# Kernel optimization log

Measured on AMD Instinct MI355X. Metric: run time of the kernel, lower is better.

Reference implementation:

```python
import jax, jax.numpy as jnp
import numpy as np

DIM = 512
NUM_HEADS = 8
HEAD_DIM = DIM // NUM_HEADS
SCALE = HEAD_DIM ** -0.5
HIDDEN = int(DIM * 4.0)
LN_EPS = 1e-5


def layer_norm(x, w, b):
    mu = jnp.mean(x, axis=-1, keepdims=True)
    var = jnp.var(x, axis=-1, keepdims=True)
    return (x - mu) * jax.lax.rsqrt(var + LN_EPS) * w + b


def setup_inputs() -> dict:
    key = jax.random.key(0)
    ks = jax.random.split(key, 8)
    s = 0.02
    return {
        "x": jax.random.normal(ks[0], (8, 4096, DIM), dtype=jnp.float32),
        "ln1_w": jnp.ones((DIM,), jnp.float32),
        "ln1_b": jnp.zeros((DIM,), jnp.float32),
        "qkv_w": jax.random.normal(ks[1], (3 * DIM, DIM), jnp.float32) * s,
        "proj_w": jax.random.normal(ks[2], (DIM, DIM), jnp.float32) * s,
        "proj_b": jnp.zeros((DIM,), jnp.float32),
        "ln2_w": jnp.ones((DIM,), jnp.float32),
        "ln2_b": jnp.zeros((DIM,), jnp.float32),
        "fc1_w": jax.random.normal(ks[3], (HIDDEN, DIM), jnp.float32) * s,
        "fc1_b": jnp.zeros((HIDDEN,), jnp.float32),
        "fc2_w": jax.random.normal(ks[4], (DIM, HIDDEN), jnp.float32) * s,
        "fc2_b": jnp.zeros((DIM,), jnp.float32),
        "eca_w": jax.random.normal(ks[5], (1, 1, 3), jnp.float32) * 0.5,
    }


def channel_attention(x, qkv_w, proj_w, proj_b):
    B, N, C = x.shape
    qkv = (x @ qkv_w.T).reshape(B, N, 3, NUM_HEADS, HEAD_DIM)
    qkv = qkv.transpose(2, 0, 3, 1, 4)  # (3, B, h, N, hd)
    q, k, v = qkv[0], qkv[1] * SCALE, qkv[2]
    # cross-covariance attention: (hd x hd) per head
    attn = jax.nn.softmax(jnp.einsum("bhnd,bhne->bhde", k, v), axis=-1)
    out = jnp.einsum("bhde,bhne->bhnd", attn, q)  # (B, h, N, hd)
    out = out.transpose(0, 2, 1, 3).reshape(B, N, C)
    return out @ proj_w.T + proj_b


def mlp_eca(x, fc1_w, fc1_b, fc2_w, fc2_b, eca_w):
    B, N, C = x.shape
    H = W = int(np.sqrt(N))
    h = jax.nn.gelu(x @ fc1_w.T + fc1_b, approximate=False)
    y = h @ fc2_w.T + fc2_b  # (B, N, C)
    # faithful replication of torch .view(B, C, H, W) on contiguous (B, N, C)
    y4 = y.reshape(B, C, H, W)
    pooled = jnp.mean(y4, axis=(2, 3))  # (B, C)
    conv = jax.lax.conv_general_dilated(
        pooled[:, None, :], eca_w, window_strides=(1,), padding=[(1, 1)],
        dimension_numbers=("NCW", "OIW", "NCW"))[:, 0, :]  # (B, C)
    gate = jax.nn.sigmoid(conv)[:, :, None, None]
    y4 = y4 * gate + y4
    return y4.reshape(B, C, H * W).transpose(0, 2, 1)  # (B, N, C)


def reference(x, ln1_w, ln1_b, qkv_w, proj_w, proj_b, ln2_w, ln2_b,
              fc1_w, fc1_b, fc2_w, fc2_b, eca_w):
    cur = layer_norm(x, ln1_w, ln1_b)
    x = x + channel_attention(cur, qkv_w, proj_w, proj_b)
    x = x + mlp_eca(layer_norm(x, ln2_w, ln2_b), fc1_w, fc1_b, fc2_w, fc2_b, eca_w)
    return x
```

## Files before the change

### kernel.cpp

```cpp
#include <hip/hip_runtime.h>
#include <hip/hip_bf16.h>

typedef __bf16 bf16;
typedef __bf16 bf16x8 __attribute__((ext_vector_type(8)));
typedef float floatx4 __attribute__((ext_vector_type(4)));

#define B_    8
#define N_    4096
#define C_    512
#define BN_   32768
#define HID_  2048
#define SCALE_ 0.125f

__device__ __forceinline__ void load_lds16(const void* g, void* l) {
    __builtin_amdgcn_global_load_lds(
        (const __attribute__((address_space(1))) void*)g,
        (__attribute__((address_space(3))) void*)l, 16, 0, 0);
}

__global__ void sniff_kernel(const unsigned int* __restrict__ xw, int* __restrict__ flag)
{
    int t = threadIdx.x;
    int votes = 0;
#pragma unroll
    for (int i = 0; i < 4; i++) {
        unsigned w = xw[t * 4 + i];
        if (w == 0u) continue;
        unsigned a = w & 0xFFFFu;
        unsigned e = (a >> 7) & 0xFFu;
        if (a != 0u && e >= 110u && e <= 135u) votes++; else votes--;
    }
#pragma unroll
    for (int off = 32; off; off >>= 1) votes += __shfl_xor(votes, off);
    __shared__ int s[4];
    if ((t & 63) == 0) s[t >> 6] = votes;
    __syncthreads();
    if (t == 0) *flag = (s[0] + s[1] + s[2] + s[3]) > 0 ? 1 : 0;
}

struct ConvArgs {
    const void* src[12];
    unsigned    dstoff[12];
    int         n[12];
};

__global__ __launch_bounds__(256) void convert_params(
    ConvArgs args, char* __restrict__ ws, const int* __restrict__ flag)
{
    int seg = blockIdx.y;
    int n = args.n[seg];
    int base = blockIdx.x * 2048;
    if (base >= n) return;
    bf16* dst = (bf16*)(ws + args.dstoff[seg]);
    const void* src = args.src[seg];
    bool isbf = (*flag != 0);
#pragma unroll
    for (int j = 0; j < 8; j++) {
        int idx = base + threadIdx.x + j * 256;
        if (idx < n) {
            float v = isbf ? (float)((const bf16*)src)[idx]
                           : ((const float*)src)[idx];
            dst[idx] = (bf16)v;
        }
    }
}

__global__ __launch_bounds__(256) void ln_dyn_kernel(
    const void* __restrict__ xv, const bf16* __restrict__ w,
    const bf16* __restrict__ b, bf16* __restrict__ out, const int* __restrict__ flag)
{
    int wave = threadIdx.x >> 6, lane = threadIdx.x & 63;
    size_t row = (size_t)blockIdx.x * 4 + wave;
    float f[8];
    if (*flag) {
        bf16x8 v = *(const bf16x8*)((const bf16*)xv + row * C_ + lane * 8);
#pragma unroll
        for (int j = 0; j < 8; j++) f[j] = (float)v[j];
    } else {
        const float4* p = (const float4*)((const float*)xv + row * C_ + lane * 8);
        float4 v0 = p[0], v1 = p[1];
        f[0]=v0.x; f[1]=v0.y; f[2]=v0.z; f[3]=v0.w;
        f[4]=v1.x; f[5]=v1.y; f[6]=v1.z; f[7]=v1.w;
    }
    float s = 0.f, sq = 0.f;
#pragma unroll
    for (int j = 0; j < 8; j++) { s += f[j]; sq += f[j]*f[j]; }
#pragma unroll
    for (int off = 32; off; off >>= 1) { s += __shfl_xor(s, off); sq += __shfl_xor(sq, off); }
    float mean = s * (1.f/512.f);
    float var  = sq * (1.f/512.f) - mean*mean;
    float inv  = rsqrtf(var + 1e-5f);
    bf16x8 wv = *(const bf16x8*)(w + lane*8);
    bf16x8 bv = *(const bf16x8*)(b + lane*8);
    bf16x8 o;
#pragma unroll
    for (int j = 0; j < 8; j++) o[j] = (bf16)((f[j]-mean)*inv*(float)wv[j] + (float)bv[j]);
    *(bf16x8*)(out + row * C_ + lane*8) = o;
}

__global__ __launch_bounds__(256) void ln_f32_kernel(
    const float* __restrict__ x, const bf16* __restrict__ w,
    const bf16* __restrict__ b, bf16* __restrict__ out)
{
    int wave = threadIdx.x >> 6, lane = threadIdx.x & 63;
    size_t row = (size_t)blockIdx.x * 4 + wave;
    const float4* p = (const float4*)(x + row * C_ + lane * 8);
    float4 v0 = p[0], v1 = p[1];
    float f[8] = { v0.x, v0.y, v0.z, v0.w, v1.x, v1.y, v1.z, v1.w };
    float s = 0.f, sq = 0.f;
#pragma unroll
    for (int j = 0; j < 8; j++) { s += f[j]; sq += f[j]*f[j]; }
#pragma unroll
    for (int off = 32; off; off >>= 1) { s += __shfl_xor(s, off); sq += __shfl_xor(sq, off); }
    float mean = s * (1.f/512.f);
    float var  = sq * (1.f/512.f) - mean*mean;
    float inv  = rsqrtf(var + 1e-5f);
    bf16x8 wv = *(const bf16x8*)(w + lane*8);
    bf16x8 bv = *(const bf16x8*)(b + lane*8);
    bf16x8 o;
#pragma unroll
    for (int j = 0; j < 8; j++) o[j] = (bf16)((f[j]-mean)*inv*(float)wv[j] + (float)bv[j]);
    *(bf16x8*)(out + row * C_ + lane*8) = o;
}

enum { EPI_NONE = 0, EPI_BIAS = 1, EPI_BIAS_RESID = 2, EPI_BIAS_GELU = 3, EPI_QKV = 4 };

template<typename OutT, int EPI>
__global__ __launch_bounds__(256, 2) void gemm_bt(
    const bf16* __restrict__ A, const bf16* __restrict__ W,
    const bf16* __restrict__ bias, const void* __restrict__ resid,
    const int* __restrict__ flag,
    OutT* __restrict__ Cout, bf16* __restrict__ Cout2, int M, int Nn, int K)
{
    __shared__ bf16 As[128][32];
    __shared__ bf16 Bs[128][32];
    const int t = threadIdx.x;
    const int wave = t >> 6, lane = t & 63;
    const int quad = lane >> 4, l16 = lane & 15;
    const int m0 = blockIdx.y * 128, n0 = blockIdx.x * 128;
    const int wm = (wave & 1) * 64, wn = (wave >> 1) * 64;
    floatx4 acc[4][4] = {};

    for (int k0 = 0; k0 < K; k0 += 32) {
#pragma unroll
        for (int i = 0; i < 2; i++) {
            int chunk = i * 256 + t;
            int row = chunk >> 2, kc = (chunk & 3) * 8;
            load_lds16(&A[(size_t)(m0 + row) * K + k0 + kc], &As[row][kc]);
            load_lds16(&W[(size_t)(n0 + row) * K + k0 + kc], &Bs[row][kc]);
        }
        __syncthreads();
        bf16x8 af[4], bfr[4];
#pragma unroll
        for (int mi = 0; mi < 4; mi++) af[mi]  = *(const bf16x8*)&As[wm + mi*16 + l16][quad*8];
#pragma unroll
        for (int ni = 0; ni < 4; ni++) bfr[ni] = *(const bf16x8*)&Bs[wn + ni*16 + l16][quad*8];
#pragma unroll
        for (int mi = 0; mi < 4; mi++)
#pragma unroll
            for (int ni = 0; ni < 4; ni++)
                acc[mi][ni] = __builtin_amdgcn_mfma_f32_16x16x32_bf16(af[mi], bfr[ni], acc[mi][ni], 0, 0, 0);
        __syncthreads();
    }

    size_t ldc = (size_t)Nn; int csub = 0; bool to2 = false;
    if (EPI == EPI_QKV) {
        if (n0 >= 512) { to2 = true; ldc = 1024; csub = 512; }
        else           { ldc = 512; }
    }
    bool isbf = false;
    if (EPI == EPI_BIAS_RESID) isbf = (*flag != 0);

#pragma unroll
    for (int mi = 0; mi < 4; mi++) {
#pragma unroll
        for (int ni = 0; ni < 4; ni++) {
            int col = n0 + wn + ni*16 + l16;
            float bv = (EPI == EPI_BIAS || EPI == EPI_BIAS_RESID || EPI == EPI_BIAS_GELU)
                       ? (float)bias[col] : 0.f;
#pragma unroll
            for (int r = 0; r < 4; r++) {
                int rowg = m0 + wm + mi*16 + quad*4 + r;
                size_t idx = (size_t)rowg * ldc + (col - csub);
                float v = acc[mi][ni][r] + bv;
                if (EPI == EPI_BIAS_RESID) {
                    float rres = isbf ? (float)((const bf16*)resid)[idx]
                                      : ((const float*)resid)[idx];
                    v += rres;
                }
                if (EPI == EPI_BIAS_GELU)  v = 0.5f * v * (1.f + erff(v * 0.70710678118654752f));
                if (EPI == EPI_QKV && to2) Cout2[idx] = (bf16)v;
                else                       Cout[idx]  = (OutT)v;
            }
        }
    }
}

__global__ __launch_bounds__(256) void attn_logits_mfma(
    const bf16* __restrict__ kv, float* __restrict__ partial)
{
    __shared__ bf16 Kt[64][136];
    __shared__ bf16 Vt[64][136];
    int s = blockIdx.x, bh = blockIdx.y, b = bh >> 3, h = bh & 7;
    int t = threadIdx.x, wave = t >> 6, lane = t & 63;
    int quad = lane >> 4, l16 = lane & 15;
    floatx4 acc[4] = {};
    for (int c = 0; c < 8; c++) {
        int n0 = s * 1024 + c * 128;
        {
            int isv = t >> 7;
            int r   = t & 127;
            const bf16* gp = &kv[((size_t)b * N_ + n0 + r) * 1024 + h * 64 + isv * 512];
            bf16x8 rowv[8];
#pragma unroll
            for (int u = 0; u < 8; u++) rowv[u] = *(const bf16x8*)(gp + u * 8);
            bf16 (*dst)[136] = isv ? Vt : Kt;
#pragma unroll
            for (int u = 0; u < 8; u++)
#pragma unroll
                for (int j = 0; j < 8; j++)
                    dst[u * 8 + j][r] = rowv[u][j];
        }
        __syncthreads();
#pragma unroll
        for (int ks = 0; ks < 4; ks++) {
            bf16x8 af = *(const bf16x8*)&Kt[wave * 16 + l16][ks * 32 + quad * 8];
#pragma unroll
            for (int ni = 0; ni < 4; ni++) {
                bf16x8 bfv = *(const bf16x8*)&Vt[ni * 16 + l16][ks * 32 + quad * 8];
                acc[ni] = __builtin_amdgcn_mfma_f32_16x16x32_bf16(af, bfv, acc[ni], 0, 0, 0);
            }
        }
        __syncthreads();
    }
    float* p = partial + ((size_t)bh * 4 + s) * 4096;
#pragma unroll
    for (int ni = 0; ni < 4; ni++)
#pragma unroll
        for (int r = 0; r < 4; r++)
            p[(wave * 16 + quad * 4 + r) * 64 + ni * 16 + l16] = acc[ni][r];
}

__global__ __launch_bounds__(256) void attn_softmax_kernel(
    const float* __restrict__ partial, bf16* __restrict__ attnb)
{
    int bh = blockIdx.x;
    int wave = threadIdx.x >> 6, lane = threadIdx.x & 63;
    for (int r = 0; r < 16; r++) {
        int d = wave * 16 + r;
        float v = 0.f;
#pragma unroll
        for (int s = 0; s < 4; s++) v += partial[((size_t)bh*4 + s)*4096 + d*64 + lane];
        v *= SCALE_;
        float m = v;
#pragma unroll
        for (int off = 32; off; off >>= 1) m = fmaxf(m, __shfl_xor(m, off));
        float p = expf(v - m);
        float sum = p;
#pragma unroll
        for (int off = 32; off; off >>= 1) sum += __shfl_xor(sum, off);
        attnb[(size_t)bh*4096 + d*64 + lane] = (bf16)(p / sum);
    }
}

__global__ __launch_bounds__(256) void attn_apply_mfma(
    const bf16* __restrict__ q, const bf16* __restrict__ attnb,
    bf16* __restrict__ outT)
{
    int bh = blockIdx.y, b = bh >> 3, h = bh & 7;
    int t = threadIdx.x, wave = t >> 6, lane = t & 63;
    int quad = lane >> 4, l16 = lane & 15;
    int nbase = blockIdx.x * 256 + wave * 64;
    bf16x8 bfrag[4][2];
#pragma unroll
    for (int di = 0; di < 4; di++)
#pragma unroll
        for (int ks = 0; ks < 2; ks++)
            bfrag[di][ks] = *(const bf16x8*)&attnb[(size_t)bh*4096 + (di*16 + l16)*64 + ks*32 + quad*8];
    floatx4 acc[4][4] = {};
#pragma unroll
    for (int mi = 0; mi < 4; mi++) {
#pragma unroll
        for (int ks = 0; ks < 2; ks++) {
            bf16x8 af = *(const bf16x8*)&q[((size_t)b*N_ + nbase + mi*16 + l16)*512 + h*64 + ks*32 + quad*8];
#pragma unroll
            for (int di = 0; di < 4; di++)
                acc[mi][di] = __builtin_amdgcn_mfma_f32_16x16x32_bf16(af, bfrag[di][ks], acc[mi][di], 0, 0, 0);
        }
    }
#pragma unroll
    for (int mi = 0; mi < 4; mi++)
#pragma unroll
        for (int di = 0; di < 4; di++)
#pragma unroll
            for (int r = 0; r < 4; r++)
                outT[((size_t)b*N_ + nbase + mi*16 + quad*4 + r)*512 + h*64 + di*16 + l16] =
                    (bf16)acc[mi][di][r];
}

__global__ __launch_bounds__(256) void pooled_kernel(
    const bf16* __restrict__ y, float* __restrict__ pooled)
{
    int bc = blockIdx.x;
    const bf16* p = y + (size_t)bc * 4096 + threadIdx.x * 16;
    float s = 0.f;
#pragma unroll
    for (int i = 0; i < 2; i++) {
        bf16x8 v = *(const bf16x8*)(p + i*8);
#pragma unroll
        for (int j = 0; j < 8; j++) s += (float)v[j];
    }
#pragma unroll
    for (int off = 32; off; off >>= 1) s += __shfl_xor(s, off);
    __shared__ float red[4];
    if ((threadIdx.x & 63) == 0) red[threadIdx.x >> 6] = s;
    __syncthreads();
    if (threadIdx.x == 0)
        pooled[bc] = (red[0] + red[1] + red[2] + red[3]) * (1.f/4096.f);
}

__global__ void gate_kernel(const float* __restrict__ pooled,
                            const bf16* __restrict__ eca_w, float* __restrict__ gate1)
{
    int c = threadIdx.x, b = blockIdx.x;
    float w0 = (float)eca_w[0], w1 = (float)eca_w[1], w2 = (float)eca_w[2];
    const float* p = pooled + b * 512;
    float conv = w1 * p[c];
    if (c > 0)   conv += w0 * p[c-1];
    if (c < 511) conv += w2 * p[c+1];
    float g = 1.f / (1.f + expf(-conv));
    gate1[b * 512 + c] = 1.f + g;
}

__global__ __launch_bounds__(256) void final_kernel(
    const bf16* __restrict__ y, const float* __restrict__ gate1,
    float* __restrict__ out)
{
    int b = blockIdx.z, c0 = blockIdx.y * 64, n0 = blockIdx.x * 64;
    __shared__ float ytile[64][65];
    int t = threadIdx.x;
#pragma unroll
    for (int i = 0; i < 2; i++) {
        int chunk = t * 2 + i;
        int ci = chunk >> 3, nj = (chunk & 7) * 8;
        bf16x8 v = *(const bf16x8*)&y[(size_t)b * ((size_t)N_*C_) + (size_t)(c0+ci) * 4096 + n0 + nj];
#pragma unroll
        for (int j = 0; j < 8; j++) ytile[ci][nj+j] = (float)v[j];
    }
    __syncthreads();
    int cc = t & 63, nb = t >> 6;
    float g = gate1[b * 512 + c0 + cc];
    for (int p = 0; p < 16; p++) {
        int nr = p * 4 + nb;
        size_t idx = ((size_t)b * N_ + n0 + nr) * C_ + c0 + cc;
        out[idx] = out[idx] + g * ytile[cc][nr];
    }
}

extern "C" void kernel_launch(void* const* d_in, const int* in_sizes, int n_in,
                              void* d_out, int out_size, void* d_ws, size_t ws_size,
                              hipStream_t stream)
{
    float* outf = (float*)d_out;
    bf16*  outb = (bf16*)d_out;
    char* ws = (char*)d_ws;

    int*   flag    = (int*)ws;
    float* pooled  = (float*)(ws + 4096);
    float* gate1   = (float*)(ws + 20480);
    bf16* ln1_w = (bf16*)(ws + 65536);
    bf16* ln1_b = (bf16*)(ws + 67584);
    bf16* ln2_w = (bf16*)(ws + 69632);
    bf16* ln2_b = (bf16*)(ws + 71680);
    bf16* proj_b= (bf16*)(ws + 73728);
    bf16* fc2_b = (bf16*)(ws + 75776);
    bf16* eca_w = (bf16*)(ws + 77824);
    bf16* fc1_b = (bf16*)(ws + 81920);
    bf16* qkv_w = (bf16*)(ws + ((size_t)1 << 20));
    bf16* proj_w= (bf16*)(ws + (size_t)2621440);
    bf16* fc1_w = (bf16*)(ws + ((size_t)3 << 20));
    bf16* fc2_w = (bf16*)(ws + ((size_t)5 << 20));
    float* partial = (float*)(ws + ((size_t)7  << 20));
    bf16*  attnb   = (bf16*)(ws + ((size_t)11 << 20));
    bf16*  T1      = (bf16*)(ws + ((size_t)16 << 20));
    bf16*  kvbuf   = (bf16*)(ws + ((size_t)48 << 20));
    bf16*  hbuf    = kvbuf;

    sniff_kernel<<<1, 256, 0, stream>>>((const unsigned int*)d_in[0], flag);

    ConvArgs ca;
    const int   srcidx[12] = { 1, 2, 6, 7, 5, 11, 12, 9, 3, 4, 8, 10 };
    const unsigned offs[12] = { 65536, 67584, 69632, 71680, 73728, 75776, 77824, 81920,
                                1u<<20, 2621440u, 3u<<20, 5u<<20 };
    for (int i = 0; i < 12; i++) {
        ca.src[i] = d_in[srcidx[i]];
        ca.dstoff[i] = offs[i];
        ca.n[i] = in_sizes[srcidx[i]];
    }
    convert_params<<<dim3(512, 12), 256, 0, stream>>>(ca, ws, flag);

    ln_dyn_kernel<<<BN_/4, 256, 0, stream>>>(d_in[0], ln1_w, ln1_b, T1, flag);

    gemm_bt<bf16, EPI_QKV><<<dim3(12, 256), 256, 0, stream>>>(
        T1, qkv_w, nullptr, nullptr, flag, outb, kvbuf, BN_, 1536, 512);

    attn_logits_mfma<<<dim3(4, 64), 256, 0, stream>>>(kvbuf, partial);
    attn_softmax_kernel<<<64, 256, 0, stream>>>(partial, attnb);
    attn_apply_mfma<<<dim3(16, 64), 256, 0, stream>>>(outb, attnb, T1);

    gemm_bt<float, EPI_BIAS_RESID><<<dim3(4, 256), 256, 0, stream>>>(
        T1, proj_w, proj_b, d_in[0], flag, outf, nullptr, BN_, 512, 512);

    ln_f32_kernel<<<BN_/4, 256, 0, stream>>>(outf, ln2_w, ln2_b, T1);

    for (int ch = 0; ch < 2; ch++) {
        bf16* Tch = T1 + (size_t)ch * 16384 * 512;
        gemm_bt<bf16, EPI_BIAS_GELU><<<dim3(16, 128), 256, 0, stream>>>(
            Tch, fc1_w, fc1_b, nullptr, flag, hbuf, nullptr, 16384, 2048, 512);
        gemm_bt<bf16, EPI_BIAS><<<dim3(4, 128), 256, 0, stream>>>(
            hbuf, fc2_w, fc2_b, nullptr, flag, Tch, nullptr, 16384, 512, 2048);
    }

    pooled_kernel<<<4096, 256, 0, stream>>>(T1, pooled);
    gate_kernel<<<8, 512, 0, stream>>>(pooled, eca_w, gate1);

    final_kernel<<<dim3(64, 8, 8), 256, 0, stream>>>(T1, gate1, outf);
}
```

Before: 581.5 us.

## Remap GEMM blocks per XCD, widen attention split, add bf16 residual path

GEMM launches move to a 1D grid whose block index is remapped so consecutive blocks on each XCD share A-row tiles, aiming for better L2 reuse. The attention logits reduction is split over 8 sequence chunks instead of 4, and the softmax uses a 2D grid, to give those small kernels more parallelism. When the workspace is large enough, the post-attention residual is kept as bf16 in a separate buffer and the MLP runs as one full-size GEMM pair instead of two halves. The final kernel then writes the output directly instead of read-modify-writing it. This cuts fp32 traffic but stores the intermediate residual at lower precision.

```diff
diff --git a/kernel.cpp b/kernel.cpp
--- a/kernel.cpp
+++ b/kernel.cpp
@@ -65,23 +65,9 @@
     }
 }
 
-__global__ __launch_bounds__(256) void ln_dyn_kernel(
-    const void* __restrict__ xv, const bf16* __restrict__ w,
-    const bf16* __restrict__ b, bf16* __restrict__ out, const int* __restrict__ flag)
-{
-    int wave = threadIdx.x >> 6, lane = threadIdx.x & 63;
-    size_t row = (size_t)blockIdx.x * 4 + wave;
-    float f[8];
-    if (*flag) {
-        bf16x8 v = *(const bf16x8*)((const bf16*)xv + row * C_ + lane * 8);
-#pragma unroll
-        for (int j = 0; j < 8; j++) f[j] = (float)v[j];
-    } else {
-        const float4* p = (const float4*)((const float*)xv + row * C_ + lane * 8);
-        float4 v0 = p[0], v1 = p[1];
-        f[0]=v0.x; f[1]=v0.y; f[2]=v0.z; f[3]=v0.w;
-        f[4]=v1.x; f[5]=v1.y; f[6]=v1.z; f[7]=v1.w;
-    }
+__device__ __forceinline__ void ln_core(float f[8], const bf16* w, const bf16* b,
+                                        int lane, bf16* outp)
+{
     float s = 0.f, sq = 0.f;
 #pragma unroll
     for (int j = 0; j < 8; j++) { s += f[j]; sq += f[j]*f[j]; }
@@ -95,7 +81,40 @@
     bf16x8 o;
 #pragma unroll
     for (int j = 0; j < 8; j++) o[j] = (bf16)((f[j]-mean)*inv*(float)wv[j] + (float)bv[j]);
-    *(bf16x8*)(out + row * C_ + lane*8) = o;
+    *(bf16x8*)outp = o;
+}
+
+__global__ __launch_bounds__(256) void ln_dyn_kernel(
+    const void* __restrict__ xv, const bf16* __restrict__ w,
+    const bf16* __restrict__ b, bf16* __restrict__ out, const int* __restrict__ flag)
+{
+    int wave = threadIdx.x >> 6, lane = threadIdx.x & 63;
+    size_t row = (size_t)blockIdx.x * 4 + wave;
+    float f[8];
+    if (*flag) {
+        bf16x8 v = *(const bf16x8*)((const bf16*)xv + row * C_ + lane * 8);
+#pragma unroll
+        for (int j = 0; j < 8; j++) f[j] = (float)v[j];
+    } else {
+        const float4* p = (const float4*)((const float*)xv + row * C_ + lane * 8);
+        float4 v0 = p[0], v1 = p[1];
+        f[0]=v0.x; f[1]=v0.y; f[2]=v0.z; f[3]=v0.w;
+        f[4]=v1.x; f[5]=v1.y; f[6]=v1.z; f[7]=v1.w;
+    }
+    ln_core(f, w, b, lane, out + row * C_ + lane*8);
+}
+
+__global__ __launch_bounds__(256) void ln_b16_kernel(
+    const bf16* __restrict__ x, const bf16* __restrict__ w,
+    const bf16* __restrict__ b, bf16* __restrict__ out)
+{
+    int wave = threadIdx.x >> 6, lane = threadIdx.x & 63;
+    size_t row = (size_t)blockIdx.x * 4 + wave;
+    bf16x8 v = *(const bf16x8*)(x + row * C_ + lane * 8);
+    float f[8];
+#pragma unroll
+    for (int j = 0; j < 8; j++) f[j] = (float)v[j];
+    ln_core(f, w, b, lane, out + row * C_ + lane*8);
 }
 
 __global__ __launch_bounds__(256) void ln_f32_kernel(
@@ -107,20 +126,7 @@
     const float4* p = (const float4*)(x + row * C_ + lane * 8);
     float4 v0 = p[0], v1 = p[1];
     float f[8] = { v0.x, v0.y, v0.z, v0.w, v1.x, v1.y, v1.z, v1.w };
-    float s = 0.f, sq = 0.f;
-#pragma unroll
-    for (int j = 0; j < 8; j++) { s += f[j]; sq += f[j]*f[j]; }
-#pragma unroll
-    for (int off = 32; off; off >>= 1) { s += __shfl_xor(s, off); sq += __shfl_xor(sq, off); }
-    float mean = s * (1.f/512.f);
-    float var  = sq * (1.f/512.f) - mean*mean;
-    float inv  = rsqrtf(var + 1e-5f);
-    bf16x8 wv = *(const bf16x8*)(w + lane*8);
-    bf16x8 bv = *(const bf16x8*)(b + lane*8);
-    bf16x8 o;
-#pragma unroll
-    for (int j = 0; j < 8; j++) o[j] = (bf16)((f[j]-mean)*inv*(float)wv[j] + (float)bv[j]);
-    *(bf16x8*)(out + row * C_ + lane*8) = o;
+    ln_core(f, w, b, lane, out + row * C_ + lane*8);
 }
 
 enum { EPI_NONE = 0, EPI_BIAS = 1, EPI_BIAS_RESID = 2, EPI_BIAS_GELU = 3, EPI_QKV = 4 };
@@ -137,7 +143,11 @@
     const int t = threadIdx.x;
     const int wave = t >> 6, lane = t & 63;
     const int quad = lane >> 4, l16 = lane & 15;
-    const int m0 = blockIdx.y * 128, n0 = blockIdx.x * 128;
+    const int Nt = Nn >> 7;
+    const int id = blockIdx.x;
+    const int xcd = id & 7, j = id >> 3;
+    const int m0 = ((j / Nt) * 8 + xcd) * 128;
+    const int n0 = (j % Nt) * 128;
     const int wm = (wave & 1) * 64, wn = (wave >> 1) * 64;
     floatx4 acc[4][4] = {};
 
@@ -205,8 +215,8 @@
     int t = threadIdx.x, wave = t >> 6, lane = t & 63;
     int quad = lane >> 4, l16 = lane & 15;
     floatx4 acc[4] = {};
-    for (int c = 0; c < 8; c++) {
-        int n0 = s * 1024 + c * 128;
+    for (int c = 0; c < 4; c++) {
+        int n0 = s * 512 + c * 128;
         {
             int isv = t >> 7;
             int r   = t & 127;
@@ -218,8 +228,8 @@
 #pragma unroll
             for (int u = 0; u < 8; u++)
 #pragma unroll
-                for (int j = 0; j < 8; j++)
-                    dst[u * 8 + j][r] = rowv[u][j];
+                for (int jj = 0; jj < 8; jj++)
+                    dst[u * 8 + jj][r] = rowv[u][jj];
         }
         __syncthreads();
 #pragma unroll
@@ -233,7 +243,7 @@
         }
         __syncthreads();
     }
-    float* p = partial + ((size_t)bh * 4 + s) * 4096;
+    float* p = partial + ((size_t)bh * 8 + s) * 4096;
 #pragma unroll
     for (int ni = 0; ni < 4; ni++)
 #pragma unroll
@@ -244,13 +254,13 @@
 __global__ __launch_bounds__(256) void attn_softmax_kernel(
     const float* __restrict__ partial, bf16* __restrict__ attnb)
 {
-    int bh = blockIdx.x;
+    int bh = blockIdx.y;
     int wave = threadIdx.x >> 6, lane = threadIdx.x & 63;
-    for (int r = 0; r < 16; r++) {
-        int d = wave * 16 + r;
+    for (int r = 0; r < 4; r++) {
+        int d = blockIdx.x * 16 + wave * 4 + r;
         float v = 0.f;
 #pragma unroll
-        for (int s = 0; s < 4; s++) v += partial[((size_t)bh*4 + s)*4096 + d*64 + lane];
+        for (int s = 0; s < 8; s++) v += partial[((size_t)bh*8 + s)*4096 + d*64 + lane];
         v *= SCALE_;
         float m = v;
 #pragma unroll
@@ -332,7 +342,7 @@
     gate1[b * 512 + c] = 1.f + g;
 }
 
-__global__ __launch_bounds__(256) void final_kernel(
+__global__ __launch_bounds__(256) void final_rmw(
     const bf16* __restrict__ y, const float* __restrict__ gate1,
     float* __restrict__ out)
 {
@@ -354,6 +364,31 @@
         int nr = p * 4 + nb;
         size_t idx = ((size_t)b * N_ + n0 + nr) * C_ + c0 + cc;
         out[idx] = out[idx] + g * ytile[cc][nr];
+    }
+}
+
+__global__ __launch_bounds__(256) void final_fresh(
+    const bf16* __restrict__ y, const bf16* __restrict__ x2b,
+    const float* __restrict__ gate1, float* __restrict__ out)
+{
+    int b = blockIdx.z, c0 = blockIdx.y * 64, n0 = blockIdx.x * 64;
+    __shared__ float ytile[64][65];
+    int t = threadIdx.x;
+#pragma unroll
+    for (int i = 0; i < 2; i++) {
+        int chunk = t * 2 + i;
+        int ci = chunk >> 3, nj = (chunk & 7) * 8;
+        bf16x8 v = *(const bf16x8*)&y[(size_t)b * ((size_t)N_*C_) + (size_t)(c0+ci) * 4096 + n0 + nj];
+#pragma unroll
+        for (int j = 0; j < 8; j++) ytile[ci][nj+j] = (float)v[j];
+    }
+    __syncthreads();
+    int cc = t & 63, nb = t >> 6;
+    float g = gate1[b * 512 + c0 + cc];
+    for (int p = 0; p < 16; p++) {
+        int nr = p * 4 + nb;
+        size_t idx = ((size_t)b * N_ + n0 + nr) * C_ + c0 + cc;
+        out[idx] = (float)x2b[idx] + g * ytile[cc][nr];
     }
 }
 
@@ -381,10 +416,13 @@
     bf16* fc1_w = (bf16*)(ws + ((size_t)3 << 20));
     bf16* fc2_w = (bf16*)(ws + ((size_t)5 << 20));
     float* partial = (float*)(ws + ((size_t)7  << 20));
-    bf16*  attnb   = (bf16*)(ws + ((size_t)11 << 20));
+    bf16*  attnb   = (bf16*)(ws + ((size_t)15 << 20));
     bf16*  T1      = (bf16*)(ws + ((size_t)16 << 20));
     bf16*  kvbuf   = (bf16*)(ws + ((size_t)48 << 20));
     bf16*  hbuf    = kvbuf;
+    bf16*  x2b     = (bf16*)(ws + ((size_t)176 << 20));
+
+    const bool fat = ws_size >= ((size_t)212 << 20);
 
     sniff_kernel<<<1, 256, 0, stream>>>((const unsigned int*)d_in[0], flag);
 
@@ -401,28 +439,37 @@
 
     ln_dyn_kernel<<<BN_/4, 256, 0, stream>>>(d_in[0], ln1_w, ln1_b, T1, flag);
 
-    gemm_bt<bf16, EPI_QKV><<<dim3(12, 256), 256, 0, stream>>>(
+    gemm_bt<bf16, EPI_QKV><<<3072, 256, 0, stream>>>(
         T1, qkv_w, nullptr, nullptr, flag, outb, kvbuf, BN_, 1536, 512);
 
-    attn_logits_mfma<<<dim3(4, 64), 256, 0, stream>>>(kvbuf, partial);
-    attn_softmax_kernel<<<64, 256, 0, stream>>>(partial, attnb);
+    attn_logits_mfma<<<dim3(8, 64), 256, 0, stream>>>(kvbuf, partial);
+    attn_softmax_kernel<<<dim3(4, 64), 256, 0, stream>>>(partial, attnb);
     attn_apply_mfma<<<dim3(16, 64), 256, 0, stream>>>(outb, attnb, T1);
 
-    gemm_bt<float, EPI_BIAS_RESID><<<dim3(4, 256), 256, 0, stream>>>(
-        T1, proj_w, proj_b, d_in[0], flag, outf, nullptr, BN_, 512, 512);
-
-    ln_f32_kernel<<<BN_/4, 256, 0, stream>>>(outf, ln2_w, ln2_b, T1);
-
-    for (int ch = 0; ch < 2; ch++) {
-        bf16* Tch = T1 + (size_t)ch * 16384 * 512;
-        gemm_bt<bf16, EPI_BIAS_GELU><<<dim3(16, 128), 256, 0, stream>>>(
-            Tch, fc1_w, fc1_b, nullptr, flag, hbuf, nullptr, 16384, 2048, 512);
-        gemm_bt<bf16, EPI_BIAS><<<dim3(4, 128), 256, 0, stream>>>(
-            hbuf, fc2_w, fc2_b, nullptr, flag, Tch, nullptr, 16384, 512, 2048);
-    }
-
-    pooled_kernel<<<4096, 256, 0, stream>>>(T1, pooled);
-    gate_kernel<<<8, 512, 0, stream>>>(pooled, eca_w, gate1);
-
-    final_kernel<<<dim3(64, 8, 8), 256, 0, stream>>>(T1, gate1, outf);
-}
+    if (fat) {
+        gemm_bt<bf16, EPI_BIAS_RESID><<<1024, 256, 0, stream>>>(
+            T1, proj_w, proj_b, d_in[0], flag, x2b, nullptr, BN_, 512, 512);
+        ln_b16_kernel<<<BN_/4, 256, 0, stream>>>(x2b, ln2_w, ln2_b, T1);
+        gemm_bt<bf16, EPI_BIAS_GELU><<<4096, 256, 0, stream>>>(
+            T1, fc1_w, fc1_b, nullptr, flag, hbuf, nullptr, BN_, 2048, 512);
+        gemm_bt<bf16, EPI_BIAS><<<1024, 256, 0, stream>>>(
+            hbuf, fc2_w, fc2_b, nullptr, flag, T1, nullptr, BN_, 512, 2048);
+        pooled_kernel<<<4096, 256, 0, stream>>>(T1, pooled);
+        gate_kernel<<<8, 512, 0, stream>>>(pooled, eca_w, gate1);
+        final_fresh<<<dim3(64, 8, 8), 256, 0, stream>>>(T1, x2b, gate1, outf);
+    } else {
+        gemm_bt<float, EPI_BIAS_RESID><<<1024, 256, 0, stream>>>(
+            T1, proj_w, proj_b, d_in[0], flag, outf, nullptr, BN_, 512, 512);
+        ln_f32_kernel<<<BN_/4, 256, 0, stream>>>(outf, ln2_w, ln2_b, T1);
+        for (int ch = 0; ch < 2; ch++) {
+            bf16* Tch = T1 + (size_t)ch * 16384 * 512;
+            gemm_bt<bf16, EPI_BIAS_GELU><<<2048, 256, 0, stream>>>(
+                Tch, fc1_w, fc1_b, nullptr, flag, hbuf, nullptr, 16384, 2048, 512);
+            gemm_bt<bf16, EPI_BIAS><<<512, 256, 0, stream>>>(
+                hbuf, fc2_w, fc2_b, nullptr, flag, Tch, nullptr, 16384, 512, 2048);
+        }
+        pooled_kernel<<<4096, 256, 0, stream>>>(T1, pooled);
+        gate_kernel<<<8, 512, 0, stream>>>(pooled, eca_w, gate1);
+        final_rmw<<<dim3(64, 8, 8), 256, 0, stream>>>(T1, gate1, outf);
+    }
+}
```

Result: faster. 542.7 us (-6.7%).
